# Kernel optimization log

Hardware: AMD Instinct MI355X
Metric: run time of the kernel (lower is better)

## Reference

```python
import jax, jax.numpy as jnp
import numpy as np

N = 100000      # nodes
E = 1600000     # edges (avg degree 16)
IN = 256        # in_channels
HID = 128       # hidden_channels
K = 10          # APPNP propagation steps
ALPHA = 0.1     # APPNP teleport probability


def setup_inputs() -> dict:
    key = jax.random.key(0)
    k1, k2, k3 = jax.random.split(key, 3)
    features = jax.random.normal(k1, (N, IN), dtype=jnp.float32)
    W = jax.random.normal(k2, (IN, HID), dtype=jnp.float32) * (1.0 / np.sqrt(IN))
    b = jnp.zeros((HID,), dtype=jnp.float32)
    edge_index = jax.random.randint(k3, (2, E), 0, N, dtype=jnp.int32)
    return {"features": features, "W": W, "b": b, "edge_index": edge_index}


def _edge_norm(src, dst, n):
    # DGL GraphConv norm='both': D_out^{-1/2} at src, D_in^{-1/2} at dst
    ones = jnp.ones(src.shape, dtype=jnp.float32)
    deg_out = jax.ops.segment_sum(ones, src, num_segments=n)
    deg_in = jax.ops.segment_sum(ones, dst, num_segments=n)
    inv_out = jnp.where(deg_out > 0, jax.lax.rsqrt(jnp.maximum(deg_out, 1.0)), 0.0)
    inv_in = jnp.where(deg_in > 0, jax.lax.rsqrt(jnp.maximum(deg_in, 1.0)), 0.0)
    return inv_out[src] * inv_in[dst]  # [E] per-edge coefficient


def _propagate(h, src, dst, enorm, n):
    # gather src features, scale by symmetric norm, scatter-add to dst
    m = h[src] * enorm[:, None]                       # [E, HID]
    return jax.ops.segment_sum(m, dst, num_segments=n)


def reference(features, W, b, edge_index):
    n = features.shape[0]
    src, dst = edge_index[0], edge_index[1]
    enorm = _edge_norm(src, dst, n)

    # GraphConv: project then aggregate (feat dropout is identity in eval)
    h = features @ W                                  # [N, HID]
    h = _propagate(h, src, dst, enorm, n) + b
    h = jax.nn.relu(h)

    # APPNP: h_{t+1} = (1-alpha) * A_hat h_t + alpha * h_0 (edge_drop off in eval)
    h0 = h

    def step(hc, _):
        hn = (1.0 - ALPHA) * _propagate(hc, src, dst, enorm, n) + ALPHA * h0
        return hn, None

    h, _ = jax.lax.scan(step, h, None, length=K)
    return h
```

## Files before the change

kernel.cpp:

```cpp
#include <hip/hip_runtime.h>
#include <hip/hip_fp16.h>
#include <stdint.h>

#define N_NODES 100000
#define N_EDGES 1600000
#define IN_CH 256
#define HID 128
#define K_STEPS 10
#define ALPHA 0.1f

#define BKT_BITS 9
#define BKT_SIZE 512
#define NBKT 196
#define HBLK 256
#define EPB (N_EDGES / HBLK)

#define DR 8
#define DRS (N_NODES / DR)
#define DC 64
#define DCE (N_EDGES / DC)

typedef _Float16 f16x8 __attribute__((ext_vector_type(8)));
typedef float f32x4 __attribute__((ext_vector_type(4)));

static __global__ __launch_bounds__(256) void bucket_hist_kernel(const int* __restrict__ dst,
                                                                 uint32_t* __restrict__ partials) {
    __shared__ uint32_t h[NBKT];
    int b = blockIdx.x, t = threadIdx.x;
    if (t < NBKT) h[t] = 0;
    __syncthreads();
    int base = b * EPB;
    for (int i = t; i < EPB; i += 256)
        atomicAdd(&h[(unsigned)dst[base + i] >> BKT_BITS], 1u);
    __syncthreads();
    if (t < NBKT) partials[t * HBLK + b] = h[t];
}

static __global__ __launch_bounds__(256) void srcdeg_hist_kernel(const int* __restrict__ src,
                                                                 uint16_t* __restrict__ srcpart) {
    __shared__ uint32_t h[DRS / 2];
    int r = blockIdx.x >> 6;
    int c = blockIdx.x & 63;
    int t = threadIdx.x;
    for (int i = t; i < DRS / 2; i += 256) h[i] = 0;
    __syncthreads();
    int lo = r * DRS;
    const int4* sp = (const int4*)(src + (size_t)c * DCE);
    for (int i = t; i < DCE / 4; i += 256) {
        int4 v = sp[i];
        unsigned a0 = (unsigned)(v.x - lo);
        unsigned a1 = (unsigned)(v.y - lo);
        unsigned a2 = (unsigned)(v.z - lo);
        unsigned a3 = (unsigned)(v.w - lo);
        if (a0 < DRS) atomicAdd(&h[a0 >> 1], 1u << ((a0 & 1) * 16));
        if (a1 < DRS) atomicAdd(&h[a1 >> 1], 1u << ((a1 & 1) * 16));
        if (a2 < DRS) atomicAdd(&h[a2 >> 1], 1u << ((a2 & 1) * 16));
        if (a3 < DRS) atomicAdd(&h[a3 >> 1], 1u << ((a3 & 1) * 16));
    }
    __syncthreads();
    uint32_t* pp = (uint32_t*)(srcpart + (size_t)c * N_NODES + lo);
    for (int i = t; i < DRS / 2; i += 256) pp[i] = h[i];
}

static __global__ void srcdeg_reduce_kernel(const uint16_t* __restrict__ srcpart,
                                            float* __restrict__ inv_out) {
    int n2 = blockIdx.x * 256 + threadIdx.x;
    if (n2 >= N_NODES / 2) return;
    uint32_t lo = 0, hi = 0;
#pragma unroll
    for (int c = 0; c < DC; c++) {
        uint32_t u = *(const uint32_t*)&srcpart[(size_t)c * N_NODES + 2 * n2];
        lo += u & 0xffffu;
        hi += u >> 16;
    }
    inv_out[2 * n2] = lo ? rsqrtf((float)lo) : 0.f;
    inv_out[2 * n2 + 1] = hi ? rsqrtf((float)hi) : 0.f;
}

static __global__ __launch_bounds__(64) void bucket_totals_kernel(const uint32_t* __restrict__ partials,
                                                                  uint32_t* __restrict__ totals) {
    int k = blockIdx.x, t = threadIdx.x;
    const uint32_t* row = partials + (size_t)k * HBLK;
    uint32_t s = row[t] + row[t + 64] + row[t + 128] + row[t + 192];
#pragma unroll
    for (int o = 32; o; o >>= 1) s += __shfl_down(s, o);
    if (t == 0) totals[k] = s;
}

static __global__ __launch_bounds__(256) void bucket_cursor_kernel(const uint32_t* __restrict__ partials,
                                                                   const uint32_t* __restrict__ totals,
                                                                   uint32_t* __restrict__ blockCursor,
                                                                   uint32_t* __restrict__ bucket_base) {
    __shared__ uint32_t sc[256];
    int k = blockIdx.x, t = threadIdx.x;
    uint32_t tk = (t < NBKT) ? totals[t] : 0;
    sc[t] = tk;
    __syncthreads();
    for (int o = 1; o < 256; o <<= 1) {
        uint32_t u = (t >= o) ? sc[t - o] : 0;
        __syncthreads();
        sc[t] += u;
        __syncthreads();
    }
    uint32_t incl_k = sc[k];
    uint32_t total_k = totals[k];
    uint32_t base = incl_k - total_k;
    if (t == 0) {
        bucket_base[k] = base;
        if (k == NBKT - 1) bucket_base[NBKT] = incl_k;
    }
    __syncthreads();
    uint32_t p = partials[(size_t)k * HBLK + t];
    sc[t] = p;
    __syncthreads();
    for (int o = 1; o < 256; o <<= 1) {
        uint32_t u = (t >= o) ? sc[t - o] : 0;
        __syncthreads();
        sc[t] += u;
        __syncthreads();
    }
    blockCursor[(size_t)k * HBLK + t] = base + sc[t] - p;
}

static __global__ __launch_bounds__(256) void bucket_scatter_kernel(const int* __restrict__ src,
                                                                    const int* __restrict__ dst,
                                                                    const uint32_t* __restrict__ blockCursor,
                                                                    int2* __restrict__ ebuf) {
    __shared__ uint32_t cur[NBKT];
    int b = blockIdx.x, t = threadIdx.x;
    if (t < NBKT) cur[t] = blockCursor[(size_t)t * HBLK + b];
    __syncthreads();
    int base = b * EPB;
    for (int i = t; i < EPB; i += 256) {
        int s = src[base + i], d = dst[base + i];
        uint32_t p = atomicAdd(&cur[(unsigned)d >> BKT_BITS], 1u);
        ebuf[p] = make_int2(s, d);
    }
}

static __global__ __launch_bounds__(256) void bucket_build_kernel(const int2* __restrict__ ebuf,
                                                                  const uint32_t* __restrict__ bucket_base,
                                                                  int* __restrict__ row_ptr,
                                                                  float* __restrict__ inv_in,
                                                                  int* __restrict__ csr) {
    __shared__ uint32_t h[BKT_SIZE];
    __shared__ uint32_t rs[BKT_SIZE];
    __shared__ uint32_t ps[256];
    int k = blockIdx.x, t = threadIdx.x;
    uint32_t b0 = bucket_base[k], b1 = bucket_base[k + 1];
    h[t] = 0; h[t + 256] = 0;
    __syncthreads();
    for (uint32_t i = b0 + t; i < b1; i += 256)
        atomicAdd(&h[ebuf[i].y & (BKT_SIZE - 1)], 1u);
    __syncthreads();
    uint32_t a = h[2 * t], bb = h[2 * t + 1];
    uint32_t pair = a + bb;
    ps[t] = pair;
    __syncthreads();
    for (int o = 1; o < 256; o <<= 1) {
        uint32_t u = (t >= o) ? ps[t - o] : 0;
        __syncthreads();
        ps[t] += u;
        __syncthreads();
    }
    uint32_t ex = ps[t] - pair;
    rs[2 * t] = ex;
    rs[2 * t + 1] = ex + a;
    int node0 = k * BKT_SIZE;
    if (node0 + 2 * t < N_NODES) {
        row_ptr[node0 + 2 * t] = (int)(b0 + ex);
        inv_in[node0 + 2 * t] = a ? rsqrtf((float)a) : 0.f;
    }
    if (node0 + 2 * t + 1 < N_NODES) {
        row_ptr[node0 + 2 * t + 1] = (int)(b0 + ex + a);
        inv_in[node0 + 2 * t + 1] = bb ? rsqrtf((float)bb) : 0.f;
    }
    if (k == NBKT - 1 && t == 0) row_ptr[N_NODES] = (int)b1;
    __syncthreads();
    for (uint32_t i = b0 + t; i < b1; i += 256) {
        int2 e = ebuf[i];
        int li = e.y & (BKT_SIZE - 1);
        uint32_t p = atomicAdd(&rs[li], 1u);
        csr[b0 + p] = e.x;
    }
}

static __global__ __launch_bounds__(256) void wtrans_kernel(const float* __restrict__ W,
                                                            _Float16* __restrict__ Wt) {
    int k = blockIdx.x * 2 + (threadIdx.x >> 7);
    int c = threadIdx.x & 127;
    Wt[(size_t)c * IN_CH + k] = (_Float16)W[(size_t)k * HID + c];
}

__device__ __forceinline__ int kswz(int row, int kb) {
    return (kb ^ ((row ^ (row >> 2)) & 3)) << 3;
}

static __global__ __launch_bounds__(256) void mfma_gemm_kernel(const float* __restrict__ A,
                                                               const _Float16* __restrict__ Wt,
                                                               const float* __restrict__ inv_out,
                                                               __half* __restrict__ t16) {
    __shared__ _Float16 As[128][32];
    __shared__ _Float16 Bs[128][32];
    __shared__ __half  Cs[128][HID];
    __shared__ float   io[128];
    int tid = threadIdx.x;
    int brow = blockIdx.x * 128;
    if (tid < 128) {
        int r = brow + tid;
        io[tid] = (r < N_NODES) ? inv_out[r] : 0.f;
    }
    int wave = tid >> 6, lane = tid & 63;
    int wm = wave >> 1, wn = wave & 1;
    int l15 = lane & 15, l4 = lane >> 4;

    f32x4 acc[4][4] = {};
    int srow = tid >> 1;
    int sko = (tid & 1) * 16;

    for (int k0 = 0; k0 < IN_CH; k0 += 32) {
        {
            float4 f[4];
            int gr = brow + srow;
            if (gr < N_NODES) {
                const float4* ap = (const float4*)&A[(size_t)gr * IN_CH + k0 + sko];
                f[0] = ap[0]; f[1] = ap[1]; f[2] = ap[2]; f[3] = ap[3];
            } else {
                f[0] = f[1] = f[2] = f[3] = make_float4(0.f, 0.f, 0.f, 0.f);
            }
#pragma unroll
            for (int g = 0; g < 2; g++) {
                _Float16 hh[8];
                float* fp = (float*)&f[2 * g];
#pragma unroll
                for (int q = 0; q < 8; q++) hh[q] = (_Float16)fp[q];
                int kb = (sko >> 3) + g;
                *(uint4*)&As[srow][kswz(srow, kb)] = *(uint4*)hh;
            }
        }
        {
            const uint4* wp = (const uint4*)&Wt[(size_t)srow * IN_CH + k0 + sko];
            uint4 u0 = wp[0], u1 = wp[1];
            int kb = sko >> 3;
            *(uint4*)&Bs[srow][kswz(srow, kb)] = u0;
            *(uint4*)&Bs[srow][kswz(srow, kb + 1)] = u1;
        }
        __syncthreads();
        f16x8 af[4], bf[4];
#pragma unroll
        for (int mt = 0; mt < 4; mt++) {
            int row = wm * 64 + mt * 16 + l15;
            af[mt] = *(f16x8*)&As[row][kswz(row, l4)];
        }
#pragma unroll
        for (int nt = 0; nt < 4; nt++) {
            int col = wn * 64 + nt * 16 + l15;
            bf[nt] = *(f16x8*)&Bs[col][kswz(col, l4)];
        }
#pragma unroll
        for (int mt = 0; mt < 4; mt++)
#pragma unroll
            for (int nt = 0; nt < 4; nt++)
                acc[mt][nt] = __builtin_amdgcn_mfma_f32_16x16x32_f16(af[mt], bf[nt], acc[mt][nt], 0, 0, 0);
        __syncthreads();
    }
#pragma unroll
    for (int mt = 0; mt < 4; mt++) {
#pragma unroll
        for (int nt = 0; nt < 4; nt++) {
#pragma unroll
            for (int r = 0; r < 4; r++) {
                int row = wm * 64 + mt * 16 + l4 * 4 + r;
                int col = wn * 64 + nt * 16 + l15;
                Cs[row][col] = __float2half(acc[mt][nt][r] * io[row]);
            }
        }
    }
    __syncthreads();
    {
        int row = tid >> 1;
        int c0 = (tid & 1) * 64;
        int gr = brow + row;
        if (gr < N_NODES) {
            uint4* s = (uint4*)&Cs[row][c0];
            uint4* d = (uint4*)&t16[(size_t)gr * HID + c0];
#pragma unroll
            for (int i = 0; i < 8; i++) d[i] = s[i];
        }
    }
}

static __global__ void zero_rows_kernel(__half* a, __half* b, __half* c) {
    int t = threadIdx.x;
    ((uint32_t*)a)[(size_t)N_NODES * 64 + t] = 0;
    ((uint32_t*)b)[(size_t)N_NODES * 64 + t] = 0;
    ((uint32_t*)c)[(size_t)N_NODES * 64 + t] = 0;
}

template <int MODE>
static __global__ __launch_bounds__(256) void prop16_kernel(const __half* __restrict__ gin,
                                                            const int* __restrict__ rp,
                                                            const int* __restrict__ cs,
                                                            const float* __restrict__ inv_in,
                                                            const float* __restrict__ inv_out,
                                                            const float* __restrict__ bias,
                                                            const __half* __restrict__ h0h,
                                                            __half* __restrict__ gout,
                                                            __half* __restrict__ h0out,
                                                            float* __restrict__ fout) {
    int wid = (int)((blockIdx.x * 256u + threadIdx.x) >> 6);
    if (wid >= N_NODES) return;
    int lane = threadIdx.x & 63;
    int sub = lane >> 4;
    int cl = lane & 15;
    int s = rp[wid], e = rp[wid + 1];
    const uint4* g4 = (const uint4*)gin;

    float a[8] = {};
    for (int j = s; j < e; j += 8) {
        int j0 = j + sub, j1 = j0 + 4;
        int v0 = cs[j0], v1 = cs[j1];
        int i0 = (j0 < e) ? v0 : N_NODES;
        int i1 = (j1 < e) ? v1 : N_NODES;
        uint4 u0 = g4[(size_t)i0 * 16 + cl];
        uint4 u1 = g4[(size_t)i1 * 16 + cl];
        const __half2* p0 = (const __half2*)&u0;
        const __half2* p1 = (const __half2*)&u1;
#pragma unroll
        for (int k = 0; k < 4; k++) {
            float2 f0 = __half22float2(p0[k]);
            float2 f1 = __half22float2(p1[k]);
            a[2 * k] += f0.x + f1.x;
            a[2 * k + 1] += f0.y + f1.y;
        }
    }
#pragma unroll
    for (int k = 0; k < 8; k++) {
        a[k] += __shfl_xor(a[k], 16);
        a[k] += __shfl_xor(a[k], 32);
    }
    if (sub != 0) return;
    int c0 = cl * 8;
    if (MODE == 0) {
        float ii = inv_in[wid], io = inv_out[wid];
        float4 b0 = *(const float4*)&bias[c0];
        float4 b1 = *(const float4*)&bias[c0 + 4];
        float h[8];
        h[0] = fmaxf(a[0] * ii + b0.x, 0.f);
        h[1] = fmaxf(a[1] * ii + b0.y, 0.f);
        h[2] = fmaxf(a[2] * ii + b0.z, 0.f);
        h[3] = fmaxf(a[3] * ii + b0.w, 0.f);
        h[4] = fmaxf(a[4] * ii + b1.x, 0.f);
        h[5] = fmaxf(a[5] * ii + b1.y, 0.f);
        h[6] = fmaxf(a[6] * ii + b1.z, 0.f);
        h[7] = fmaxf(a[7] * ii + b1.w, 0.f);
        __half2 hh[4], gg[4];
#pragma unroll
        for (int k = 0; k < 4; k++) {
            hh[k] = __floats2half2_rn(h[2 * k], h[2 * k + 1]);
            gg[k] = __floats2half2_rn(h[2 * k] * io, h[2 * k + 1] * io);
        }
        ((uint4*)h0out)[(size_t)wid * 16 + cl] = *(uint4*)hh;
        ((uint4*)gout)[(size_t)wid * 16 + cl] = *(uint4*)gg;
    } else {
        float ii = inv_in[wid] * (1.f - ALPHA);
        uint4 uh = ((const uint4*)h0h)[(size_t)wid * 16 + cl];
        const __half2* ph = (const __half2*)&uh;
        float h[8];
#pragma unroll
        for (int k = 0; k < 4; k++) {
            float2 f = __half22float2(ph[k]);
            h[2 * k] = a[2 * k] * ii + ALPHA * f.x;
            h[2 * k + 1] = a[2 * k + 1] * ii + ALPHA * f.y;
        }
        if (MODE == 1) {
            float io = inv_out[wid];
            __half2 gg[4];
#pragma unroll
            for (int k = 0; k < 4; k++)
                gg[k] = __floats2half2_rn(h[2 * k] * io, h[2 * k + 1] * io);
            ((uint4*)gout)[(size_t)wid * 16 + cl] = *(uint4*)gg;
        } else {
            *(float4*)&fout[(size_t)wid * HID + c0] = make_float4(h[0], h[1], h[2], h[3]);
            *(float4*)&fout[(size_t)wid * HID + c0 + 4] = make_float4(h[4], h[5], h[6], h[7]);
        }
    }
}

extern "C" void kernel_launch(void* const* d_in, const int* in_sizes, int n_in,
                              void* d_out, int out_size, void* d_ws, size_t ws_size,
                              hipStream_t stream) {
    const float* features = (const float*)d_in[0];
    const float* W = (const float*)d_in[1];
    const float* b = (const float*)d_in[2];
    const int* edge_index = (const int*)d_in[3];
    const int* src = edge_index;
    const int* dst = edge_index + N_EDGES;
    float* out = (float*)d_out;

    char* ws = (char*)d_ws;
    size_t off = 0;
    auto alloc = [&](size_t bytes) -> void* {
        void* p = ws + off;
        off = (off + bytes + 255) & ~(size_t)255;
        return p;
    };
    int* csr = (int*)alloc(((size_t)N_EDGES + 8) * 4);
    __half* t16 = (__half*)alloc((size_t)(N_NODES + 1) * HID * 2);
    __half* gA  = (__half*)alloc((size_t)(N_NODES + 1) * HID * 2);
    __half* gB  = (__half*)alloc((size_t)(N_NODES + 1) * HID * 2);
    __half* h0h = (__half*)alloc((size_t)N_NODES * HID * 2);
    float* inv_out = (float*)alloc((size_t)N_NODES * 4);
    float* inv_in = (float*)alloc((size_t)N_NODES * 4);
    int* row_ptr = (int*)alloc((size_t)(N_NODES + 1) * 4);
    _Float16* Wt = (_Float16*)alloc((size_t)HID * IN_CH * 2);
    char* tb = (char*)gA;
    size_t toff = 0;
    auto talloc = [&](size_t bytes) -> void* {
        void* p = tb + toff;
        toff = (toff + bytes + 255) & ~(size_t)255;
        return p;
    };
    int2* ebuf = (int2*)talloc((size_t)N_EDGES * 8);
    uint16_t* srcpart = (uint16_t*)talloc((size_t)DC * N_NODES * 2);
    uint32_t* partials = (uint32_t*)talloc((size_t)NBKT * HBLK * 4);
    uint32_t* blockCursor = (uint32_t*)talloc((size_t)NBKT * HBLK * 4);
    uint32_t* totals = (uint32_t*)talloc(NBKT * 4);
    uint32_t* bucket_base = (uint32_t*)talloc((NBKT + 1) * 4);

    bucket_hist_kernel<<<HBLK, 256, 0, stream>>>(dst, partials);
    srcdeg_hist_kernel<<<DR * DC, 256, 0, stream>>>(src, srcpart);
    srcdeg_reduce_kernel<<<(N_NODES / 2 + 255) / 256, 256, 0, stream>>>(srcpart, inv_out);
    bucket_totals_kernel<<<NBKT, 64, 0, stream>>>(partials, totals);
    bucket_cursor_kernel<<<NBKT, 256, 0, stream>>>(partials, totals, blockCursor, bucket_base);
    bucket_scatter_kernel<<<HBLK, 256, 0, stream>>>(src, dst, blockCursor, ebuf);
    bucket_build_kernel<<<NBKT, 256, 0, stream>>>(ebuf, bucket_base, row_ptr, inv_in, csr);

    wtrans_kernel<<<128, 256, 0, stream>>>(W, Wt);
    mfma_gemm_kernel<<<(N_NODES + 127) / 128, 256, 0, stream>>>(features, Wt, inv_out, t16);
    zero_rows_kernel<<<1, 64, 0, stream>>>(t16, gA, gB);

    int pb = (int)(((size_t)N_NODES * 64) / 256);
    prop16_kernel<0><<<pb, 256, 0, stream>>>(t16, row_ptr, csr, inv_in, inv_out, b, nullptr,
                                             gA, h0h, nullptr);
    const __half* cur = gA;
    for (int t = 0; t < K_STEPS - 1; t++) {
        __half* nxt = (t & 1) ? gA : gB;
        prop16_kernel<1><<<pb, 256, 0, stream>>>(cur, row_ptr, csr, inv_in, inv_out, nullptr, h0h,
                                                 nxt, nullptr, nullptr);
        cur = nxt;
    }
    prop16_kernel<2><<<pb, 256, 0, stream>>>(cur, row_ptr, csr, inv_in, inv_out, nullptr, h0h,
                                             nullptr, nullptr, out);
}
```

Measured before the change: 796.2 us.

## Slice feature buffers into column chunks and propagate per slice with persistent warps

```diff
diff --git a/kernel.cpp b/kernel.cpp
--- a/kernel.cpp
+++ b/kernel.cpp
@@ -19,6 +19,11 @@
 #define DRS (N_NODES / DR)
 #define DC 64
 #define DCE (N_EDGES / DC)
+
+#define NSLICE 8
+#define PROP_BLOCKS 2048
+#define WPS 1024
+#define NPW ((N_NODES + WPS - 1) / WPS)
 
 typedef _Float16 f16x8 __attribute__((ext_vector_type(8)));
 typedef float f32x4 __attribute__((ext_vector_type(4)));
@@ -279,110 +284,99 @@
     __syncthreads();
     {
         int row = tid >> 1;
-        int c0 = (tid & 1) * 64;
+        int h64 = tid & 1;
         int gr = brow + row;
         if (gr < N_NODES) {
-            uint4* s = (uint4*)&Cs[row][c0];
-            uint4* d = (uint4*)&t16[(size_t)gr * HID + c0];
-#pragma unroll
-            for (int i = 0; i < 8; i++) d[i] = s[i];
-        }
-    }
-}
-
-static __global__ void zero_rows_kernel(__half* a, __half* b, __half* c) {
-    int t = threadIdx.x;
-    ((uint32_t*)a)[(size_t)N_NODES * 64 + t] = 0;
-    ((uint32_t*)b)[(size_t)N_NODES * 64 + t] = 0;
-    ((uint32_t*)c)[(size_t)N_NODES * 64 + t] = 0;
+#pragma unroll
+            for (int g = 0; g < 4; g++) {
+                int si = h64 * 4 + g;
+                uint4* sp = (uint4*)&Cs[row][h64 * 64 + g * 16];
+                uint4* dp = (uint4*)(t16 + ((size_t)si * N_NODES + gr) * 16);
+                dp[0] = sp[0];
+                dp[1] = sp[1];
+            }
+        }
+    }
 }
 
 template <int MODE>
-static __global__ __launch_bounds__(256) void prop16_kernel(const __half* __restrict__ gin,
-                                                            const int* __restrict__ rp,
-                                                            const int* __restrict__ cs,
-                                                            const float* __restrict__ inv_in,
-                                                            const float* __restrict__ inv_out,
-                                                            const float* __restrict__ bias,
-                                                            const __half* __restrict__ h0h,
-                                                            __half* __restrict__ gout,
-                                                            __half* __restrict__ h0out,
-                                                            float* __restrict__ fout) {
-    int wid = (int)((blockIdx.x * 256u + threadIdx.x) >> 6);
-    if (wid >= N_NODES) return;
+static __global__ __launch_bounds__(256, 8) void prop_slice_kernel(const _Float16* __restrict__ gin,
+                                                                   const int* __restrict__ rp,
+                                                                   const int* __restrict__ cs,
+                                                                   const float* __restrict__ inv_in,
+                                                                   const float* __restrict__ inv_out,
+                                                                   const float* __restrict__ bias,
+                                                                   const _Float16* __restrict__ h0s,
+                                                                   _Float16* __restrict__ gout,
+                                                                   _Float16* __restrict__ h0out,
+                                                                   float* __restrict__ fout) {
+    int s = blockIdx.x & 7;
+    int wslice = (blockIdx.x >> 3) * 4 + (threadIdx.x >> 6);
     int lane = threadIdx.x & 63;
-    int sub = lane >> 4;
-    int cl = lane & 15;
-    int s = rp[wid], e = rp[wid + 1];
-    const uint4* g4 = (const uint4*)gin;
-
-    float a[8] = {};
-    for (int j = s; j < e; j += 8) {
-        int j0 = j + sub, j1 = j0 + 4;
-        int v0 = cs[j0], v1 = cs[j1];
-        int i0 = (j0 < e) ? v0 : N_NODES;
-        int i1 = (j1 < e) ? v1 : N_NODES;
-        uint4 u0 = g4[(size_t)i0 * 16 + cl];
-        uint4 u1 = g4[(size_t)i1 * 16 + cl];
-        const __half2* p0 = (const __half2*)&u0;
-        const __half2* p1 = (const __half2*)&u1;
-#pragma unroll
-        for (int k = 0; k < 4; k++) {
-            float2 f0 = __half22float2(p0[k]);
-            float2 f1 = __half22float2(p1[k]);
-            a[2 * k] += f0.x + f1.x;
-            a[2 * k + 1] += f0.y + f1.y;
-        }
-    }
-#pragma unroll
-    for (int k = 0; k < 8; k++) {
-        a[k] += __shfl_xor(a[k], 16);
-        a[k] += __shfl_xor(a[k], 32);
-    }
-    if (sub != 0) return;
-    int c0 = cl * 8;
-    if (MODE == 0) {
-        float ii = inv_in[wid], io = inv_out[wid];
-        float4 b0 = *(const float4*)&bias[c0];
-        float4 b1 = *(const float4*)&bias[c0 + 4];
-        float h[8];
-        h[0] = fmaxf(a[0] * ii + b0.x, 0.f);
-        h[1] = fmaxf(a[1] * ii + b0.y, 0.f);
-        h[2] = fmaxf(a[2] * ii + b0.z, 0.f);
-        h[3] = fmaxf(a[3] * ii + b0.w, 0.f);
-        h[4] = fmaxf(a[4] * ii + b1.x, 0.f);
-        h[5] = fmaxf(a[5] * ii + b1.y, 0.f);
-        h[6] = fmaxf(a[6] * ii + b1.z, 0.f);
-        h[7] = fmaxf(a[7] * ii + b1.w, 0.f);
-        __half2 hh[4], gg[4];
-#pragma unroll
-        for (int k = 0; k < 4; k++) {
-            hh[k] = __floats2half2_rn(h[2 * k], h[2 * k + 1]);
-            gg[k] = __floats2half2_rn(h[2 * k] * io, h[2 * k + 1] * io);
-        }
-        ((uint4*)h0out)[(size_t)wid * 16 + cl] = *(uint4*)hh;
-        ((uint4*)gout)[(size_t)wid * 16 + cl] = *(uint4*)gg;
-    } else {
-        float ii = inv_in[wid] * (1.f - ALPHA);
-        uint4 uh = ((const uint4*)h0h)[(size_t)wid * 16 + cl];
-        const __half2* ph = (const __half2*)&uh;
-        float h[8];
-#pragma unroll
-        for (int k = 0; k < 4; k++) {
-            float2 f = __half22float2(ph[k]);
-            h[2 * k] = a[2 * k] * ii + ALPHA * f.x;
-            h[2 * k + 1] = a[2 * k + 1] * ii + ALPHA * f.y;
-        }
-        if (MODE == 1) {
-            float io = inv_out[wid];
-            __half2 gg[4];
-#pragma unroll
-            for (int k = 0; k < 4; k++)
-                gg[k] = __floats2half2_rn(h[2 * k] * io, h[2 * k + 1] * io);
-            ((uint4*)gout)[(size_t)wid * 16 + cl] = *(uint4*)gg;
-        } else {
-            *(float4*)&fout[(size_t)wid * HID + c0] = make_float4(h[0], h[1], h[2], h[3]);
-            *(float4*)&fout[(size_t)wid * HID + c0 + 4] = make_float4(h[4], h[5], h[6], h[7]);
+    int sub = lane >> 2;
+    int cl = lane & 3;
+    const uint2* gsl = (const uint2*)(gin + (size_t)s * N_NODES * 16);
+    const uint64_t* h0p = (const uint64_t*)(h0s + (size_t)s * N_NODES * 16);
+    uint64_t* gop = (uint64_t*)(gout + (size_t)s * N_NODES * 16);
+    uint64_t* h0op = (uint64_t*)(h0out + (size_t)s * N_NODES * 16);
+
+    int n0 = wslice * NPW;
+    int n1 = n0 + NPW;
+    if (n1 > N_NODES) n1 = N_NODES;
+    for (int wid = n0; wid < n1; ++wid) {
+        int rs = rp[wid], re = rp[wid + 1];
+        float a0 = 0.f, a1 = 0.f, a2 = 0.f, a3 = 0.f;
+        for (int j = rs + sub; j < re; j += 16) {
+            int idx = __builtin_nontemporal_load(cs + j);
+            uint2 u = gsl[(size_t)idx * 4 + cl];
+            float2 f01 = __half22float2(*(__half2*)&u.x);
+            float2 f23 = __half22float2(*(__half2*)&u.y);
+            a0 += f01.x; a1 += f01.y; a2 += f23.x; a3 += f23.y;
+        }
+#pragma unroll
+        for (int m = 4; m <= 32; m <<= 1) {
+            a0 += __shfl_xor(a0, m);
+            a1 += __shfl_xor(a1, m);
+            a2 += __shfl_xor(a2, m);
+            a3 += __shfl_xor(a3, m);
+        }
+        if (lane < 4) {
+            int c0 = s * 16 + cl * 4;
+            if (MODE == 0) {
+                float ii = inv_in[wid], io = inv_out[wid];
+                float4 bb = *(const float4*)&bias[c0];
+                float h0v = fmaxf(a0 * ii + bb.x, 0.f);
+                float h1v = fmaxf(a1 * ii + bb.y, 0.f);
+                float h2v = fmaxf(a2 * ii + bb.z, 0.f);
+                float h3v = fmaxf(a3 * ii + bb.w, 0.f);
+                __half2 p01 = __floats2half2_rn(h0v, h1v);
+                __half2 p23 = __floats2half2_rn(h2v, h3v);
+                uint64_t uh = ((uint64_t)(*(uint32_t*)&p23) << 32) | (*(uint32_t*)&p01);
+                __builtin_nontemporal_store(uh, h0op + (size_t)wid * 4 + cl);
+                __half2 g01 = __floats2half2_rn(h0v * io, h1v * io);
+                __half2 g23 = __floats2half2_rn(h2v * io, h3v * io);
+                uint64_t ug = ((uint64_t)(*(uint32_t*)&g23) << 32) | (*(uint32_t*)&g01);
+                __builtin_nontemporal_store(ug, gop + (size_t)wid * 4 + cl);
+            } else {
+                float ii = inv_in[wid] * (1.f - ALPHA);
+                uint64_t uh = __builtin_nontemporal_load(h0p + (size_t)wid * 4 + cl);
+                uint32_t hlo = (uint32_t)uh, hhi = (uint32_t)(uh >> 32);
+                float2 f01 = __half22float2(*(__half2*)&hlo);
+                float2 f23 = __half22float2(*(__half2*)&hhi);
+                float h0v = a0 * ii + ALPHA * f01.x;
+                float h1v = a1 * ii + ALPHA * f01.y;
+                float h2v = a2 * ii + ALPHA * f23.x;
+                float h3v = a3 * ii + ALPHA * f23.y;
+                if (MODE == 1) {
+                    float io = inv_out[wid];
+                    __half2 g01 = __floats2half2_rn(h0v * io, h1v * io);
+                    __half2 g23 = __floats2half2_rn(h2v * io, h3v * io);
+                    uint64_t ug = ((uint64_t)(*(uint32_t*)&g23) << 32) | (*(uint32_t*)&g01);
+                    __builtin_nontemporal_store(ug, gop + (size_t)wid * 4 + cl);
+                } else {
+                    *(float4*)&fout[(size_t)wid * HID + c0] = make_float4(h0v, h1v, h2v, h3v);
+                }
+            }
         }
     }
 }
@@ -406,10 +400,10 @@
         return p;
     };
     int* csr = (int*)alloc(((size_t)N_EDGES + 8) * 4);
-    __half* t16 = (__half*)alloc((size_t)(N_NODES + 1) * HID * 2);
-    __half* gA  = (__half*)alloc((size_t)(N_NODES + 1) * HID * 2);
-    __half* gB  = (__half*)alloc((size_t)(N_NODES + 1) * HID * 2);
-    __half* h0h = (__half*)alloc((size_t)N_NODES * HID * 2);
+    _Float16* t16 = (_Float16*)alloc((size_t)NSLICE * N_NODES * 16 * 2);
+    _Float16* gA  = (_Float16*)alloc((size_t)NSLICE * N_NODES * 16 * 2);
+    _Float16* gB  = (_Float16*)alloc((size_t)NSLICE * N_NODES * 16 * 2);
+    _Float16* h0s = (_Float16*)alloc((size_t)NSLICE * N_NODES * 16 * 2);
     float* inv_out = (float*)alloc((size_t)N_NODES * 4);
     float* inv_in = (float*)alloc((size_t)N_NODES * 4);
     int* row_ptr = (int*)alloc((size_t)(N_NODES + 1) * 4);
@@ -437,19 +431,17 @@
     bucket_build_kernel<<<NBKT, 256, 0, stream>>>(ebuf, bucket_base, row_ptr, inv_in, csr);
 
     wtrans_kernel<<<128, 256, 0, stream>>>(W, Wt);
-    mfma_gemm_kernel<<<(N_NODES + 127) / 128, 256, 0, stream>>>(features, Wt, inv_out, t16);
-    zero_rows_kernel<<<1, 64, 0, stream>>>(t16, gA, gB);
-
-    int pb = (int)(((size_t)N_NODES * 64) / 256);
-    prop16_kernel<0><<<pb, 256, 0, stream>>>(t16, row_ptr, csr, inv_in, inv_out, b, nullptr,
-                                             gA, h0h, nullptr);
-    const __half* cur = gA;
+    mfma_gemm_kernel<<<(N_NODES + 127) / 128, 256, 0, stream>>>(features, Wt, inv_out, (__half*)t16);
+
+    prop_slice_kernel<0><<<PROP_BLOCKS, 256, 0, stream>>>(t16, row_ptr, csr, inv_in, inv_out, b,
+                                                          nullptr, gA, h0s, nullptr);
+    const _Float16* cur = gA;
     for (int t = 0; t < K_STEPS - 1; t++) {
-        __half* nxt = (t & 1) ? gA : gB;
-        prop16_kernel<1><<<pb, 256, 0, stream>>>(cur, row_ptr, csr, inv_in, inv_out, nullptr, h0h,
-                                                 nxt, nullptr, nullptr);
+        _Float16* nxt = (t & 1) ? gA : gB;
+        prop_slice_kernel<1><<<PROP_BLOCKS, 256, 0, stream>>>(cur, row_ptr, csr, inv_in, inv_out,
+                                                              nullptr, h0s, nxt, nullptr, nullptr);
         cur = nxt;
     }
-    prop16_kernel<2><<<pb, 256, 0, stream>>>(cur, row_ptr, csr, inv_in, inv_out, nullptr, h0h,
-                                             nullptr, nullptr, out);
-}
+    prop_slice_kernel<2><<<PROP_BLOCKS, 256, 0, stream>>>(cur, row_ptr, csr, inv_in, inv_out,
+                                                          nullptr, h0s, nullptr, nullptr, out);
+}
```

Result: slower. 3.030 ms (+280.6%).
